# Kernel tuning notes

Measured on AMD Instinct MI355X. Metric: run time of the kernel, lower is better.

Reference implementation:

```python
import jax, jax.numpy as jnp
import numpy as np

D, H, BS, K_TOP = 2560, 32, 32, 16
HD = D // H  # 80
B, S = 2, 1024
SCALE = HD ** -0.5


def setup_inputs() -> dict:
    key = jax.random.key(0)
    ks = jax.random.split(key, 10)
    sc = 0.02

    def lin(k, i, o):
        return (jax.random.normal(k, (i, o), jnp.float32) * sc,
                jnp.zeros((o,), jnp.float32))

    Wq, bq = lin(ks[0], D, D)
    Wk, bk = lin(ks[1], D, D)
    Wv, bv = lin(ks[2], D, D)
    Wo, bo = lin(ks[3], D, D)
    comp_W1, comp_b1 = lin(ks[4], BS * HD, 4 * HD)
    comp_W2, comp_b2 = lin(ks[5], 4 * HD, HD)
    comp_pos = jax.random.normal(ks[6], (BS, HD), jnp.float32) * sc
    gate_W1, gate_b1 = lin(ks[7], D, D // 2)
    gate_W2, gate_b2 = lin(ks[8], D // 2, 3)
    hidden_states = jax.random.normal(ks[9], (B, S, D), jnp.float32)
    return dict(hidden_states=hidden_states, Wq=Wq, bq=bq, Wk=Wk, bk=bk,
                Wv=Wv, bv=bv, Wo=Wo, bo=bo, comp_pos=comp_pos,
                comp_W1=comp_W1, comp_b1=comp_b1, comp_W2=comp_W2,
                comp_b2=comp_b2, gate_W1=gate_W1, gate_b1=gate_b1,
                gate_W2=gate_W2, gate_b2=gate_b2)


def reference(hidden_states, Wq, bq, Wk, bk, Wv, bv, Wo, bo, comp_pos,
              comp_W1, comp_b1, comp_W2, comp_b2, gate_W1, gate_b1,
              gate_W2, gate_b2):
    b, s, dm = hidden_states.shape
    blocks = s // BS

    def heads(y):  # [b,s,D] -> [b,H,s,hd]
        return y.reshape(b, s, H, HD).transpose(0, 2, 1, 3)

    q = heads(hidden_states @ Wq + bq)
    k = heads(hidden_states @ Wk + bk)
    v = heads(hidden_states @ Wv + bv)

    # --- compression branch: per-head block compression MLP (shared K/V) ---
    def compress(t):  # [b,H,s,hd] -> [b,H,blocks,hd]
        tb = t.reshape(b, H, blocks, BS, HD) + comp_pos  # pos emb per block slot
        tb = tb.reshape(b, H, blocks, BS * HD)
        h1 = jax.nn.gelu(tb @ comp_W1 + comp_b1, approximate=False)
        return h1 @ comp_W2 + comp_b2

    kc = compress(k)
    vc = compress(v)
    attn_c = jax.nn.softmax(jnp.einsum('bhsd,bhnd->bhsn', q, kc) * SCALE, axis=-1)
    out_c = jnp.einsum('bhsn,bhnd->bhsd', attn_c, vc)

    # --- dense scores, shared by selection scoring and window branch ---
    scores = jnp.einsum('bhqd,bhkd->bhqk', q, k) * SCALE  # [b,H,s,s]

    # --- selection branch: per-query top-k blocks by block-mean score ---
    block_scores = scores.reshape(b, H, s, blocks, BS).mean(-1)  # [b,H,s,blocks]
    _, top_idx = jax.lax.top_k(block_scores, K_TOP)  # [b,H,s,K]
    sel = (jnp.arange(blocks)[None, None, None, None, :] == top_idx[..., None]).any(-2)
    key_mask = jnp.repeat(sel, BS, axis=-1)  # [b,H,s,s]
    sel_scores = jnp.where(key_mask, scores, -jnp.inf)
    out_s = jnp.einsum('bhqk,bhkd->bhqd', jax.nn.softmax(sel_scores, axis=-1), v)

    # --- window branch: source's window mask is all-ones -> full attention ---
    out_w = jnp.einsum('bhqk,bhkd->bhqd', jax.nn.softmax(scores, axis=-1), v)

    # --- learned gates ---
    gh = jax.nn.gelu(hidden_states @ gate_W1 + gate_b1, approximate=False)
    gates = jax.nn.sigmoid(gh @ gate_W2 + gate_b2)  # [b,s,3]
    g = gates.transpose(2, 0, 1)[:, :, None, :, None]  # [3,b,1,s,1]
    combined = g[0] * out_c + g[1] * out_s + g[2] * out_w  # [b,H,s,hd]
    combined = combined.transpose(0, 2, 1, 3).reshape(b, s, dm)
    return combined @ Wo + bo
```

## Files before the change

kernel.cpp:

```cpp
#include <hip/hip_runtime.h>
#include <hip/hip_bf16.h>
#include <math.h>

typedef unsigned short u16;
typedef short v8s __attribute__((ext_vector_type(8)));
typedef float v4f __attribute__((ext_vector_type(4)));

#define SCALE_F 0.11180339887498949f
#define SCALE_L2 0.16129821534f

__device__ __forceinline__ float bf2f(u16 x) {
    unsigned int u = ((unsigned int)x) << 16;
    return __builtin_bit_cast(float, u);
}
__device__ __forceinline__ u16 f2bf(float f) {
    unsigned int u = __builtin_bit_cast(unsigned int, f);
    unsigned int r = (u + 0x7FFFu + ((u >> 16) & 1u)) >> 16;
    return (u16)r;
}
__device__ __forceinline__ float scrub(float v) {
    return (fabsf(v) < 1e30f) ? v : 0.f;
}
__device__ __forceinline__ v8s zero8() {
    union { v8s v; short s[8]; } t;
#pragma unroll
    for (int i = 0; i < 8; i++) t.s[i] = 0;
    return t.v;
}
__device__ __forceinline__ void glds16(const void* g, void* s) {
    __builtin_amdgcn_global_load_lds(
        (const __attribute__((address_space(1))) unsigned int*)g,
        (__attribute__((address_space(3))) unsigned int*)s, 16, 0, 0);
}

__global__ void convX_kernel(const float* __restrict__ X, u16* __restrict__ Xb, int n)
{
    int i = (blockIdx.x * 256 + threadIdx.x) * 4;
    if (i >= n) return;
    float4 v = *(const float4*)(X + i);
    u16 o[4] = { f2bf(v.x), f2bf(v.y), f2bf(v.z), f2bf(v.w) };
    *(uint2*)(Xb + i) = *(uint2*)o;
}

__global__ __launch_bounds__(256) void convT_kernel(
    const float* __restrict__ W, u16* __restrict__ WT, int K, int N)
{
    __shared__ float t[32][33];
    int n0 = blockIdx.x * 32, k0 = blockIdx.y * 32;
    int tx = threadIdx.x & 31, ty = threadIdx.x >> 5;
    for (int i = ty; i < 32; i += 8) {
        int k = k0 + i, n = n0 + tx;
        t[i][tx] = (k < K && n < N) ? W[(size_t)k * N + n] : 0.f;
    }
    __syncthreads();
    for (int i = ty; i < 32; i += 8) {
        int n = n0 + i, k = k0 + tx;
        if (n < N && k < K) WT[(size_t)n * K + k] = f2bf(t[tx][i]);
    }
}

__global__ void xmean_kernel(const float* __restrict__ X, float* __restrict__ Xm)
{
    int c = blockIdx.x * 256 + threadIdx.x;
    if (c >= 2560) return;
    int g = blockIdx.y;
    const float* base = X + (size_t)g * 32 * 2560 + c;
    float s = 0.f;
#pragma unroll 4
    for (int j = 0; j < 32; j++) s += base[(size_t)j * 2560];
    Xm[(size_t)g * 2560 + c] = s * (1.f / 32.f);
}

__global__ __launch_bounds__(256) void gemmS_kernel(
    const float* __restrict__ A, const float* __restrict__ B,
    const float* __restrict__ bias, int M, int N, int K, float* __restrict__ outf)
{
    __shared__ __align__(16) u16 Ah[64][32], Al[64][32];
    __shared__ __align__(16) u16 Bh[64][32], Bl[64][32];
    const int tid = threadIdx.x;
    const int bm = blockIdx.x * 64, bn = blockIdx.y * 64;
    const int w = tid >> 6, lane = tid & 63;
    const int quad = lane >> 4, l = lane & 15;
    v4f acc[4];
#pragma unroll
    for (int nt = 0; nt < 4; nt++)
#pragma unroll
        for (int r = 0; r < 4; r++) acc[nt][r] = 0.f;
    const int ar = tid >> 2, ak = (tid & 3) * 8;
    const int kr = tid >> 3, nc = (tid & 7) * 8;
    for (int k0 = 0; k0 < K; k0 += 32) {
        float4 a0 = *(const float4*)(A + (size_t)(bm + ar) * K + (k0 + ak));
        float4 a1 = *(const float4*)(A + (size_t)(bm + ar) * K + (k0 + ak) + 4);
        float4 b0 = *(const float4*)(B + (size_t)(k0 + kr) * N + (bn + nc));
        float4 b1 = *(const float4*)(B + (size_t)(k0 + kr) * N + (bn + nc) + 4);
        float av[8] = {a0.x,a0.y,a0.z,a0.w,a1.x,a1.y,a1.z,a1.w};
        float bv[8] = {b0.x,b0.y,b0.z,b0.w,b1.x,b1.y,b1.z,b1.w};
        __syncthreads();
#pragma unroll
        for (int j = 0; j < 8; j++) {
            u16 h = f2bf(av[j]);
            Ah[ar][ak + j] = h; Al[ar][ak + j] = f2bf(av[j] - bf2f(h));
            u16 g = f2bf(bv[j]);
            Bh[nc + j][kr] = g; Bl[nc + j][kr] = f2bf(bv[j] - bf2f(g));
        }
        __syncthreads();
        v8s ah = *(const v8s*)(&Ah[w * 16 + l][quad * 8]);
        v8s al = *(const v8s*)(&Al[w * 16 + l][quad * 8]);
#pragma unroll
        for (int nt = 0; nt < 4; nt++) {
            v8s bh = *(const v8s*)(&Bh[nt * 16 + l][quad * 8]);
            v8s bl = *(const v8s*)(&Bl[nt * 16 + l][quad * 8]);
            acc[nt] = __builtin_amdgcn_mfma_f32_16x16x32_bf16(ah, bh, acc[nt], 0, 0, 0);
            acc[nt] = __builtin_amdgcn_mfma_f32_16x16x32_bf16(ah, bl, acc[nt], 0, 0, 0);
            acc[nt] = __builtin_amdgcn_mfma_f32_16x16x32_bf16(al, bh, acc[nt], 0, 0, 0);
        }
    }
#pragma unroll
    for (int nt = 0; nt < 4; nt++) {
        int col = bn + nt * 16 + l;
        float bvs = bias[col];
#pragma unroll
        for (int r = 0; r < 4; r++) {
            int row = bm + w * 16 + quad * 4 + r;
            outf[(size_t)row * N + col] = scrub(acc[nt][r] + bvs);
        }
    }
}

__global__ __launch_bounds__(256) void m1_kernel(
    const float* __restrict__ Wq, const float* __restrict__ km,
    u16* __restrict__ M1hT, u16* __restrict__ M1lT)
{
    __shared__ float Ws[64][81];
    __shared__ float Ks[32][80];
    int k0 = blockIdx.x * 64, h = blockIdx.y, b = blockIdx.z;
    int tid = threadIdx.x;
    for (int i = tid; i < 64 * 80; i += 256) {
        int kk = i / 80, dd = i - kk * 80;
        Ws[kk][dd] = Wq[(size_t)(k0 + kk) * 2560 + h * 80 + dd];
    }
    for (int i = tid; i < 32 * 80; i += 256) {
        int bl = i / 80, dd = i - bl * 80;
        Ks[bl][dd] = km[(size_t)((b << 5) + bl) * 2560 + h * 80 + dd];
    }
    __syncthreads();
    int kk = tid & 63, bq4 = tid >> 6;
    for (int bt = 0; bt < 8; bt++) {
        int blk = bt * 4 + bq4;
        float s = 0.f;
#pragma unroll 8
        for (int d = 0; d < 80; d++) s += Ws[kk][d] * Ks[blk][d];
        u16 hi = f2bf(s);
        size_t o = (size_t)(b * 1024 + h * 32 + blk) * 2560 + k0 + kk;
        M1hT[o] = hi;
        M1lT[o] = f2bf(s - bf2f(hi));
    }
}

__global__ void bias3_kernel(const float* __restrict__ bq, const float* __restrict__ km,
                             float* __restrict__ bias3)
{
    int i = blockIdx.x * 256 + threadIdx.x;
    if (i >= 2048) return;
    int b = i >> 10, hb = i & 1023, h = hb >> 5, blk = hb & 31;
    float s = 0.f;
    for (int d = 0; d < 80; d++) s += bq[h * 80 + d] * km[(size_t)((b << 5) + blk) * 2560 + h * 80 + d];
    bias3[i] = s;
}

__global__ __launch_bounds__(256) void gemmS2_kernel(
    const float* __restrict__ A, const u16* __restrict__ BhT, const u16* __restrict__ BlT,
    const float* __restrict__ bias, int M, int N, int K, float* __restrict__ outf)
{
    __shared__ __align__(16) u16 Ah[2][64][32], Al[2][64][32];
    __shared__ __align__(16) u16 Bh[2][64][32], Bl[2][64][32];
    const int tid = threadIdx.x;
    const int z = blockIdx.z;
    const float* Az = A + (size_t)z * 1024 * 2560;
    const u16* Bhz = BhT + (size_t)z * 1024 * 2560;
    const u16* Blz = BlT + (size_t)z * 1024 * 2560;
    const float* biasz = bias + (size_t)z * 1024;
    float* outz = outf + (size_t)z * 1024 * 1024;
    const int bm = blockIdx.x * 64, bn = blockIdx.y * 64;
    const int w = tid >> 6, lane = tid & 63;
    const int quad = lane >> 4, l = lane & 15;
    v4f acc[4];
#pragma unroll
    for (int nt = 0; nt < 4; nt++)
#pragma unroll
        for (int r = 0; r < 4; r++) acc[nt][r] = 0.f;
    const int ar = tid >> 2, ak = (tid & 3) * 8;
    const float* ApF = Az + (size_t)(bm + ar) * K + ak;
    const u16* BpH = Bhz + (size_t)(bn + ar) * K + ak;
    const u16* BpL = Blz + (size_t)(bn + ar) * K + ak;
    char* BhB = (char*)Bh;
    char* BlB = (char*)Bl;
    const int NT = K >> 5;
    glds16(BpH, BhB + w * 1024);
    glds16(BpL, BlB + w * 1024);
    float4 a0 = *(const float4*)(ApF);
    float4 a1 = *(const float4*)(ApF + 4);
    __syncthreads();
    for (int t = 0; t < NT; t++) {
        const int cur = t & 1;
        const int nxt = cur ^ 1;
        if (t + 1 < NT) {
            int k0n = (t + 1) << 5;
            glds16(BpH + k0n, BhB + nxt * 4096 + w * 1024);
            glds16(BpL + k0n, BlB + nxt * 4096 + w * 1024);
        }
        float av[8] = {a0.x, a0.y, a0.z, a0.w, a1.x, a1.y, a1.z, a1.w};
        if (t + 1 < NT) {
            int k0n = (t + 1) << 5;
            a0 = *(const float4*)(ApF + k0n);
            a1 = *(const float4*)(ApF + k0n + 4);
        }
#pragma unroll
        for (int j = 0; j < 8; j++) {
            u16 h = f2bf(av[j]);
            Ah[cur][ar][ak + j] = h;
            Al[cur][ar][ak + j] = f2bf(av[j] - bf2f(h));
        }
        v8s ah = *(const v8s*)(&Ah[cur][w * 16 + l][quad * 8]);
        v8s al2 = *(const v8s*)(&Al[cur][w * 16 + l][quad * 8]);
#pragma unroll
        for (int nt = 0; nt < 4; nt++) {
            v8s bh = *(const v8s*)(&Bh[cur][nt * 16 + l][quad * 8]);
            v8s bl = *(const v8s*)(&Bl[cur][nt * 16 + l][quad * 8]);
            acc[nt] = __builtin_amdgcn_mfma_f32_16x16x32_bf16(ah, bh, acc[nt], 0, 0, 0);
            acc[nt] = __builtin_amdgcn_mfma_f32_16x16x32_bf16(ah, bl, acc[nt], 0, 0, 0);
            acc[nt] = __builtin_amdgcn_mfma_f32_16x16x32_bf16(al2, bh, acc[nt], 0, 0, 0);
        }
        __syncthreads();
    }
#pragma unroll
    for (int nt = 0; nt < 4; nt++) {
        int col = bn + nt * 16 + l;
        float bvs = biasz[col];
#pragma unroll
        for (int r = 0; r < 4; r++) {
            int row = bm + w * 16 + quad * 4 + r;
            outz[(size_t)row * N + col] = scrub(acc[nt][r] + bvs);
        }
    }
}

__global__ __launch_bounds__(256) void gemmB_kernel(
    const u16* __restrict__ A, const u16* __restrict__ Al2, const u16* __restrict__ BT,
    const float* __restrict__ bias, int M, int N, int K, int act, int ldc,
    u16* __restrict__ outb, float* __restrict__ outf, u16* __restrict__ outT)
{
    __shared__ __align__(16) u16 As[2][64][32];
    __shared__ __align__(16) u16 As2[2][64][32];
    __shared__ __align__(16) u16 Bs[2][64][32];
    const int tid = threadIdx.x;
    const int bm = blockIdx.x * 64, bn = blockIdx.y * 64;
    const int w = tid >> 6, lane = tid & 63;
    const int quad = lane >> 4, l = lane & 15;
    v4f acc[4];
#pragma unroll
    for (int nt = 0; nt < 4; nt++)
#pragma unroll
        for (int r = 0; r < 4; r++) acc[nt][r] = 0.f;
    const int srow = w * 16 + (lane >> 2);
    const int kcol = (lane & 3) * 8;
    const int brow = (bn + srow < N) ? (bn + srow) : (N - 1);
    const u16* Ap = A + (size_t)(bm + srow) * K + kcol;
    const u16* Bp = BT + (size_t)brow * K + kcol;
    const u16* A2p = Al2 ? (Al2 + (size_t)(bm + srow) * K + kcol) : nullptr;
    char* AsB = (char*)As;
    char* As2B = (char*)As2;
    char* BsB = (char*)Bs;
    const int NT = K >> 5;
    glds16(Ap, AsB + w * 1024);
    glds16(Bp, BsB + w * 1024);
    if (Al2) glds16(A2p, As2B + w * 1024);
    __syncthreads();
    for (int t = 0; t < NT; t++) {
        const int cur = t & 1;
        const int nxt = cur ^ 1;
        if (t + 1 < NT) {
            int k0n = (t + 1) << 5;
            glds16(Ap + k0n, AsB + nxt * 4096 + w * 1024);
            glds16(Bp + k0n, BsB + nxt * 4096 + w * 1024);
            if (Al2) glds16(A2p + k0n, As2B + nxt * 4096 + w * 1024);
        }
        v8s af = *(const v8s*)(&As[cur][w * 16 + l][quad * 8]);
#pragma unroll
        for (int nt = 0; nt < 4; nt++) {
            v8s bf = *(const v8s*)(&Bs[cur][nt * 16 + l][quad * 8]);
            acc[nt] = __builtin_amdgcn_mfma_f32_16x16x32_bf16(af, bf, acc[nt], 0, 0, 0);
        }
        if (Al2) {
            v8s af2 = *(const v8s*)(&As2[cur][w * 16 + l][quad * 8]);
#pragma unroll
            for (int nt = 0; nt < 4; nt++) {
                v8s bf = *(const v8s*)(&Bs[cur][nt * 16 + l][quad * 8]);
                acc[nt] = __builtin_amdgcn_mfma_f32_16x16x32_bf16(af2, bf, acc[nt], 0, 0, 0);
            }
        }
        __syncthreads();
    }
#pragma unroll
    for (int nt = 0; nt < 4; nt++) {
        int col = bn + nt * 16 + l;
        if (col < N) {
            float bvs = bias[col];
#pragma unroll
            for (int r = 0; r < 4; r++) {
                int row = bm + w * 16 + quad * 4 + r;
                float c = acc[nt][r] + bvs;
                if (act == 1) c = 0.5f * c * (1.0f + erff(c * 0.70710678118654752f));
                c = scrub(c);
                if (outf) outf[(size_t)row * ldc + col] = c;
                if (outb) outb[(size_t)row * ldc + col] = f2bf(c);
                if (outT) {
                    int bb = row >> 10, s = row & 1023;
                    int hh = col / 80, dd = col - hh * 80;
                    outT[((size_t)((bb << 5) + hh) * 96 + dd) * 1024 + s] = f2bf(c);
                }
            }
        }
    }
}

__global__ void gatherF_kernel(const u16* __restrict__ src, const float* __restrict__ pos,
                               u16* __restrict__ F)
{
    int row = blockIdx.y;
    int col = blockIdx.x * 256 + threadIdx.x;
    if (col >= 2560) return;
    int b = row >> 10, h = (row >> 5) & 31, blk = row & 31;
    int j = col / 80, d = col - j * 80;
    float v = bf2f(src[(size_t)(b * 1024 + blk * 32 + j) * 2560 + h * 80 + d]) + pos[col];
    F[(size_t)row * 2560 + col] = f2bf(v);
}
__global__ void gatherFT_kernel(const u16* __restrict__ vt, const float* __restrict__ pos,
                                u16* __restrict__ F)
{
    int row = blockIdx.y;
    int col = blockIdx.x * 256 + threadIdx.x;
    if (col >= 2560) return;
    int b = row >> 10, h = (row >> 5) & 31, blk = row & 31;
    int j = col / 80, d = col - j * 80;
    float v = bf2f(vt[((size_t)((b << 5) + h) * 96 + d) * 1024 + blk * 32 + j]) + pos[col];
    F[(size_t)row * 2560 + col] = f2bf(v);
}

__global__ __launch_bounds__(256) void gates_kernel(
    const u16* __restrict__ gh, const float* __restrict__ W2,
    const float* __restrict__ b2, float* __restrict__ gates)
{
    int w = threadIdx.x >> 6, lane = threadIdx.x & 63;
    int token = blockIdx.x * 4 + w;
    float s0 = 0.f, s1 = 0.f, s2 = 0.f;
    for (int i = lane; i < 1280; i += 64) {
        float g = bf2f(gh[(size_t)token * 1280 + i]);
        s0 += g * W2[i * 3 + 0];
        s1 += g * W2[i * 3 + 1];
        s2 += g * W2[i * 3 + 2];
    }
#pragma unroll
    for (int m = 1; m < 64; m <<= 1) {
        s0 += __shfl_xor(s0, m);
        s1 += __shfl_xor(s1, m);
        s2 += __shfl_xor(s2, m);
    }
    if (lane == 0) {
        gates[token * 3 + 0] = scrub(1.f / (1.f + expf(-(s0 + b2[0]))));
        gates[token * 3 + 1] = scrub(1.f / (1.f + expf(-(s1 + b2[1]))));
        gates[token * 3 + 2] = scrub(1.f / (1.f + expf(-(s2 + b2[2]))));
    }
}

__global__ __launch_bounds__(64) void attn_kernel(
    const u16* __restrict__ qb, const u16* __restrict__ kbf,
    const u16* __restrict__ vt, const u16* __restrict__ kc,
    const u16* __restrict__ vc, const float* __restrict__ BSf,
    const float* __restrict__ gates, u16* __restrict__ comb, u16* __restrict__ combl)
{
    const int lane = threadIdx.x, quad = lane >> 4, l = lane & 15;
    const int qt = blockIdx.x, bh = blockIdx.y, b = bh >> 5, h = bh & 31;
    const float NEG = -1e30f;

    __shared__ float bs[16][33];
    __shared__ unsigned int selmask[16];
    __shared__ __align__(16) u16 Pw[16][40];
    __shared__ float ocn[16][80];

    {
        const float* bsrow = BSf + ((size_t)b * 1024 + qt * 16 + l) * 1024 + h * 32 + quad * 8;
#pragma unroll
        for (int i = 0; i < 8; i++) bs[l][quad * 8 + i] = bsrow[i] * SCALE_F;
    }
    __syncthreads();
    if (lane < 16) {
        unsigned int mask = 0u;
        for (int it = 0; it < 16; it++) {
            float best = NEG; int bi = -1;
            for (int n = 0; n < 32; n++) {
                if (((mask >> n) & 1u) == 0u && bs[lane][n] > best) { best = bs[lane][n]; bi = n; }
            }
            if (bi < 0) { for (int n = 0; n < 32; n++) if (((mask >> n) & 1u) == 0u) { bi = n; break; } }
            mask |= (1u << bi);
        }
        selmask[lane] = mask;
    }
    __syncthreads();
    const unsigned int selm_l = selmask[l];
    unsigned int selm[4];
#pragma unroll
    for (int r = 0; r < 4; r++) selm[r] = selmask[quad * 4 + r];

    v8s qfrag[3];
    {
        const u16* qrow = qb + (size_t)(b * 1024 + qt * 16 + l) * 2560 + h * 80;
#pragma unroll
        for (int c = 0; c < 3; c++) {
            if (c == 2 && quad >= 2) { qfrag[c] = zero8(); }
            else qfrag[c] = *(const v8s*)(qrow + c * 32 + quad * 8);
        }
    }

    {
        v4f oc[5];
#pragma unroll
        for (int t = 0; t < 5; t++)
#pragma unroll
            for (int r = 0; r < 4; r++) oc[t][r] = 0.f;
        float l_c[4];
        v4f s0, s1;
#pragma unroll
        for (int r = 0; r < 4; r++) { s0[r] = 0.f; s1[r] = 0.f; }
#pragma unroll
        for (int c = 0; c < 3; c++) {
            v8s b0, b1;
            if (c == 2 && quad >= 2) { b0 = zero8(); b1 = zero8(); }
            else {
                b0 = *(const v8s*)(kc + (size_t)(bh * 32 + l) * 80 + c * 32 + quad * 8);
                b1 = *(const v8s*)(kc + (size_t)(bh * 32 + 16 + l) * 80 + c * 32 + quad * 8);
            }
            s0 = __builtin_amdgcn_mfma_f32_16x16x32_bf16(qfrag[c], b0, s0, 0, 0, 0);
            s1 = __builtin_amdgcn_mfma_f32_16x16x32_bf16(qfrag[c], b1, s1, 0, 0, 0);
        }
#pragma unroll
        for (int r = 0; r < 4; r++) {
            float x0 = s0[r] * SCALE_L2, x1 = s1[r] * SCALE_L2;
            float mx = fmaxf(x0, x1);
#pragma unroll
            for (int m = 1; m < 16; m <<= 1) mx = fmaxf(mx, __shfl_xor(mx, m));
            float p0 = exp2f(x0 - mx), p1 = exp2f(x1 - mx);
            float sm = p0 + p1;
#pragma unroll
            for (int m = 1; m < 16; m <<= 1) sm += __shfl_xor(sm, m);
            l_c[r] = sm;
            Pw[quad * 4 + r][l]      = f2bf(p0);
            Pw[quad * 4 + r][l + 16] = f2bf(p1);
        }
        __syncthreads();
        v8s pa = *(const v8s*)(&Pw[l][quad * 8]);
#pragma unroll
        for (int t = 0; t < 5; t++) {
            union { v8s v; short s[8]; } vf;
#pragma unroll
            for (int j = 0; j < 8; j++)
                vf.s[j] = (short)vc[(size_t)(bh * 32 + quad * 8 + j) * 80 + t * 16 + l];
            oc[t] = __builtin_amdgcn_mfma_f32_16x16x32_bf16(pa, vf.v, oc[t], 0, 0, 0);
        }
#pragma unroll
        for (int r = 0; r < 4; r++) {
            int token = b * 1024 + qt * 16 + quad * 4 + r;
            float g0 = gates[token * 3 + 0];
            float fc = g0 / fmaxf(l_c[r], 1e-30f);
#pragma unroll
            for (int t = 0; t < 5; t++) ocn[quad * 4 + r][t * 16 + l] = oc[t][r] * fc;
        }
        __syncthreads();
    }

    v4f aw[5], as_[5];
    float m_w[4], l_w[4], l_s[4];
#pragma unroll
    for (int r = 0; r < 4; r++) { m_w[r] = NEG; l_w[r] = 0.f; l_s[r] = 0.f; }
#pragma unroll
    for (int t = 0; t < 5; t++)
#pragma unroll
        for (int r = 0; r < 4; r++) { aw[t][r] = 0.f; as_[t][r] = 0.f; }

    const u16* vtp = vt + (size_t)bh * 96 * 1024;

    for (int kb = 0; kb < 32; kb++) {
        v4f s0, s1;
#pragma unroll
        for (int r = 0; r < 4; r++) { s0[r] = 0.f; s1[r] = 0.f; }
#pragma unroll
        for (int c = 0; c < 3; c++) {
            v8s k0f, k1f;
            if (c == 2 && quad >= 2) { k0f = zero8(); k1f = zero8(); }
            else {
                size_t base = (size_t)(b * 1024 + kb * 32) * 2560 + h * 80 + c * 32 + quad * 8;
                k0f = *(const v8s*)(kbf + base + (size_t)l * 2560);
                k1f = *(const v8s*)(kbf + base + (size_t)(16 + l) * 2560);
            }
            s0 = __builtin_amdgcn_mfma_f32_16x16x32_bf16(qfrag[c], k0f, s0, 0, 0, 0);
            s1 = __builtin_amdgcn_mfma_f32_16x16x32_bf16(qfrag[c], k1f, s1, 0, 0, 0);
        }
        float x0a[4], x1a[4], pmax[4];
        float needmax = NEG;
#pragma unroll
        for (int r = 0; r < 4; r++) {
            x0a[r] = s0[r] * SCALE_L2; x1a[r] = s1[r] * SCALE_L2;
            float mb = fmaxf(x0a[r], x1a[r]);
#pragma unroll
            for (int m = 1; m < 16; m <<= 1) mb = fmaxf(mb, __shfl_xor(mb, m));
            pmax[r] = mb;
            needmax = fmaxf(needmax, mb - m_w[r]);
        }
        if (__all(needmax <= 8.0f)) {
#pragma unroll
            for (int r = 0; r < 4; r++) {
                float p0 = exp2f(x0a[r] - m_w[r]), p1 = exp2f(x1a[r] - m_w[r]);
                Pw[quad * 4 + r][l]      = f2bf(p0);
                Pw[quad * 4 + r][l + 16] = f2bf(p1);
                float st = p0 + p1;
#pragma unroll
                for (int m = 1; m < 16; m <<= 1) st += __shfl_xor(st, m);
                l_w[r] += st;
                if ((selm[r] >> kb) & 1u) l_s[r] += st;
            }
        } else {
            float alw[4];
#pragma unroll
            for (int r = 0; r < 4; r++) {
                float mn = fmaxf(m_w[r], pmax[r]);
                alw[r] = exp2f(m_w[r] - mn);
                m_w[r] = mn;
                float p0 = exp2f(x0a[r] - mn), p1 = exp2f(x1a[r] - mn);
                Pw[quad * 4 + r][l]      = f2bf(p0);
                Pw[quad * 4 + r][l + 16] = f2bf(p1);
                float st = p0 + p1;
#pragma unroll
                for (int m = 1; m < 16; m <<= 1) st += __shfl_xor(st, m);
                l_w[r] = l_w[r] * alw[r] + st;
                l_s[r] = l_s[r] * alw[r] + (((selm[r] >> kb) & 1u) ? st : 0.f);
            }
#pragma unroll
            for (int t = 0; t < 5; t++)
#pragma unroll
                for (int r = 0; r < 4; r++) { aw[t][r] *= alw[r]; as_[t][r] *= alw[r]; }
        }
        __syncthreads();
        v8s pwa = *(const v8s*)(&Pw[l][quad * 8]);
        v8s psa = ((selm_l >> kb) & 1u) ? pwa : zero8();
#pragma unroll
        for (int t = 0; t < 5; t++) {
            v8s vfr = *(const v8s*)(vtp + ((size_t)(t * 16 + l)) * 1024 + kb * 32 + quad * 8);
            aw[t]  = __builtin_amdgcn_mfma_f32_16x16x32_bf16(pwa, vfr, aw[t], 0, 0, 0);
            as_[t] = __builtin_amdgcn_mfma_f32_16x16x32_bf16(psa, vfr, as_[t], 0, 0, 0);
        }
        __syncthreads();
    }

#pragma unroll
    for (int r = 0; r < 4; r++) {
        int token = b * 1024 + qt * 16 + quad * 4 + r;
        float g1 = gates[token * 3 + 1], g2 = gates[token * 3 + 2];
        float fw = g2 / fmaxf(l_w[r], 1e-30f);
        float fs = g1 / fmaxf(l_s[r], 1e-30f);
#pragma unroll
        for (int t = 0; t < 5; t++) {
            float val = ocn[quad * 4 + r][t * 16 + l] + fs * as_[t][r] + fw * aw[t][r];
            val = scrub(val);
            u16 hi = f2bf(val);
            size_t o = (size_t)token * 2560 + h * 80 + t * 16 + l;
            comb[o] = hi;
            combl[o] = f2bf(val - bf2f(hi));
        }
    }
}

extern "C" void kernel_launch(void* const* d_in, const int* in_sizes, int n_in,
                              void* d_out, int out_size, void* d_ws, size_t ws_size,
                              hipStream_t stream)
{
    (void)in_sizes; (void)n_in; (void)out_size; (void)ws_size;

    const float* X   = (const float*)d_in[0];
    const float* Wq  = (const float*)d_in[1];
    const float* bq  = (const float*)d_in[2];
    const float* Wk  = (const float*)d_in[3];
    const float* bk  = (const float*)d_in[4];
    const float* Wv  = (const float*)d_in[5];
    const float* bv  = (const float*)d_in[6];
    const float* Wo  = (const float*)d_in[7];
    const float* bo  = (const float*)d_in[8];
    const float* pos = (const float*)d_in[9];
    const float* cW1 = (const float*)d_in[10];
    const float* cb1 = (const float*)d_in[11];
    const float* cW2 = (const float*)d_in[12];
    const float* cb2 = (const float*)d_in[13];
    const float* gW1 = (const float*)d_in[14];
    const float* gb1 = (const float*)d_in[15];
    const float* gW2 = (const float*)d_in[16];
    const float* gb2 = (const float*)d_in[17];

    char* ws = (char*)d_ws;
    size_t off = 0;
    auto alloc = [&](size_t bytes) -> void* {
        void* p = ws + off;
        off += (bytes + 255) & ~(size_t)255;
        return p;
    };
    u16*   Xb     = (u16*)  alloc(2048ull * 2560 * 2);
    u16*   WqT    = (u16*)  alloc(2560ull * 2560 * 2);
    u16*   WkT    = (u16*)  alloc(2560ull * 2560 * 2);
    u16*   WvT    = (u16*)  alloc(2560ull * 2560 * 2);
    u16*   WoT    = (u16*)  alloc(2560ull * 2560 * 2);
    u16*   gW1T   = (u16*)  alloc(1280ull * 2560 * 2);
    u16*   cW1T   = (u16*)  alloc(320ull * 2560 * 2);
    u16*   cW2T   = (u16*)  alloc(96ull * 320 * 2);
    float* Xm     = (float*)alloc(64ull * 2560 * 4);
    float* kmeanS = (float*)alloc(64ull * 2560 * 4);
    u16*   M1hT   = (u16*)  alloc(2048ull * 2560 * 2);
    u16*   M1lT   = (u16*)  alloc(2048ull * 2560 * 2);
    float* bias3  = (float*)alloc(2048ull * 4);
    u16*   qbuf   = (u16*)  alloc(2048ull * 2560 * 2);
    u16*   kbf    = (u16*)  alloc(2048ull * 2560 * 2);
    u16*   vtb    = (u16*)  alloc(64ull * 96 * 1024 * 2);
    u16*   combl  = (u16*)  alloc(2048ull * 2560 * 2);
    char*  R1     = (char*) alloc(12ull * 1024 * 1024);
    u16*   gh     = (u16*)R1;
    u16*   Fb     = (u16*)R1;
    u16*   H1     = (u16*)(R1 + 10ull * 1024 * 1024);
    u16*   combb  = (u16*)R1;
    u16*   KC     = (u16*)  alloc(2048ull * 80 * 2);
    u16*   VC     = (u16*)  alloc(2048ull * 80 * 2);
    float* gatesf = (float*)alloc(2048ull * 3 * 4);
    float* BSf    = (float*)d_out;

    dim3 blk(256);
    convX_kernel<<<2048 * 2560 / 4 / 256, blk, 0, stream>>>(X, Xb, 2048 * 2560);
    convT_kernel<<<dim3(80, 80), blk, 0, stream>>>(Wq, WqT, 2560, 2560);
    convT_kernel<<<dim3(80, 80), blk, 0, stream>>>(Wk, WkT, 2560, 2560);
    convT_kernel<<<dim3(80, 80), blk, 0, stream>>>(Wv, WvT, 2560, 2560);
    convT_kernel<<<dim3(80, 80), blk, 0, stream>>>(Wo, WoT, 2560, 2560);
    convT_kernel<<<dim3(40, 80), blk, 0, stream>>>(gW1, gW1T, 2560, 1280);
    convT_kernel<<<dim3(10, 80), blk, 0, stream>>>(cW1, cW1T, 2560, 320);
    convT_kernel<<<dim3(3, 10), blk, 0, stream>>>(cW2, cW2T, 320, 80);
    xmean_kernel<<<dim3(10, 64), blk, 0, stream>>>(X, Xm);
    gemmS_kernel<<<dim3(1, 40), blk, 0, stream>>>(Xm, Wk, bk, 64, 2560, 2560, kmeanS);
    m1_kernel<<<dim3(40, 32, 2), blk, 0, stream>>>(Wq, kmeanS, M1hT, M1lT);
    bias3_kernel<<<8, blk, 0, stream>>>(bq, kmeanS, bias3);
    gemmS2_kernel<<<dim3(16, 16, 2), blk, 0, stream>>>(X, M1hT, M1lT, bias3, 1024, 1024, 2560, BSf);
    gemmB_kernel<<<dim3(32, 40), blk, 0, stream>>>(Xb, nullptr, WqT, bq, 2048, 2560, 2560, 0, 2560, qbuf, nullptr, nullptr);
    gemmB_kernel<<<dim3(32, 40), blk, 0, stream>>>(Xb, nullptr, WkT, bk, 2048, 2560, 2560, 0, 2560, kbf, nullptr, nullptr);
    gemmB_kernel<<<dim3(32, 40), blk, 0, stream>>>(Xb, nullptr, WvT, bv, 2048, 2560, 2560, 0, 2560, nullptr, nullptr, vtb);
    gemmB_kernel<<<dim3(32, 20), blk, 0, stream>>>(Xb, nullptr, gW1T, gb1, 2048, 1280, 2560, 1, 1280, gh, nullptr, nullptr);
    gates_kernel<<<512, blk, 0, stream>>>(gh, gW2, gb2, gatesf);
    gatherF_kernel<<<dim3(10, 2048), blk, 0, stream>>>(kbf, pos, Fb);
    gemmB_kernel<<<dim3(32, 5), blk, 0, stream>>>(Fb, nullptr, cW1T, cb1, 2048, 320, 2560, 1, 320, H1, nullptr, nullptr);
    gemmB_kernel<<<dim3(32, 2), blk, 0, stream>>>(H1, nullptr, cW2T, cb2, 2048, 80, 320, 0, 80, KC, nullptr, nullptr);
    gatherFT_kernel<<<dim3(10, 2048), blk, 0, stream>>>(vtb, pos, Fb);
    gemmB_kernel<<<dim3(32, 5), blk, 0, stream>>>(Fb, nullptr, cW1T, cb1, 2048, 320, 2560, 1, 320, H1, nullptr, nullptr);
    gemmB_kernel<<<dim3(32, 2), blk, 0, stream>>>(H1, nullptr, cW2T, cb2, 2048, 80, 320, 0, 80, VC, nullptr, nullptr);
    attn_kernel<<<dim3(64, 64), 64, 0, stream>>>(qbuf, kbf, vtb, KC, VC, BSf, gatesf, combb, combl);
    gemmB_kernel<<<dim3(32, 40), blk, 0, stream>>>(combb, combl, WoT, bo, 2048, 2560, 2560, 0, 2560, nullptr, (float*)d_out, nullptr);
}
```

Baseline: 1.137 ms.

## Software-pipeline K loads, hoist V loads, and drop single-wavefront barriers in attention

The attention key loop is unrolled by two with ping-pong register buffers, so the K fragments for the next block are loaded while the current block's softmax runs. The five V fragments are issued at the start of each iteration, ahead of the QK MFMAs. Every __syncthreads is removed on the basis that the block is a single 64-lane wavefront. This is meant to hide global-memory latency and cut barrier overhead, at the cost of more live registers and a reliance on implicit wavefront-level ordering of LDS accesses.

```diff
diff --git a/kernel.cpp b/kernel.cpp
--- a/kernel.cpp
+++ b/kernel.cpp
@@ -373,6 +373,94 @@
     }
 }
 
+#define KLOAD(K0,K1,K2,K3,K4,K5, kbv) do {                                    \
+    size_t base_ = (size_t)(b * 1024 + (kbv) * 32) * 2560 + h * 80 + quad * 8;\
+    const u16* p0_ = kbf + base_ + (size_t)l * 2560;                          \
+    const u16* p1_ = kbf + base_ + (size_t)(16 + l) * 2560;                   \
+    K0 = *(const v8s*)(p0_);                                                  \
+    K1 = *(const v8s*)(p0_ + 32);                                             \
+    K3 = *(const v8s*)(p1_);                                                  \
+    K4 = *(const v8s*)(p1_ + 32);                                             \
+    if (quad < 2) { K2 = *(const v8s*)(p0_ + 64); K5 = *(const v8s*)(p1_ + 64); } \
+    else { K2 = zero8(); K5 = zero8(); }                                      \
+} while (0)
+
+#define ATTN_ITER(kbv, K0,K1,K2,K3,K4,K5, DOPRE, N0,N1,N2,N3,N4,N5) do {      \
+    const int kb_ = (kbv);                                                    \
+    const u16* vp_ = vtp + kb_ * 32 + quad * 8;                               \
+    v8s va0_ = *(const v8s*)(vp_ + (size_t)(l) * 1024);                       \
+    v8s va1_ = *(const v8s*)(vp_ + (size_t)(16 + l) * 1024);                  \
+    v8s va2_ = *(const v8s*)(vp_ + (size_t)(32 + l) * 1024);                  \
+    v8s va3_ = *(const v8s*)(vp_ + (size_t)(48 + l) * 1024);                  \
+    v8s va4_ = *(const v8s*)(vp_ + (size_t)(64 + l) * 1024);                  \
+    v4f s0_, s1_;                                                             \
+    _Pragma("unroll")                                                         \
+    for (int r = 0; r < 4; r++) { s0_[r] = 0.f; s1_[r] = 0.f; }               \
+    s0_ = __builtin_amdgcn_mfma_f32_16x16x32_bf16(qfrag[0], K0, s0_, 0, 0, 0);\
+    s0_ = __builtin_amdgcn_mfma_f32_16x16x32_bf16(qfrag[1], K1, s0_, 0, 0, 0);\
+    s0_ = __builtin_amdgcn_mfma_f32_16x16x32_bf16(qfrag[2], K2, s0_, 0, 0, 0);\
+    s1_ = __builtin_amdgcn_mfma_f32_16x16x32_bf16(qfrag[0], K3, s1_, 0, 0, 0);\
+    s1_ = __builtin_amdgcn_mfma_f32_16x16x32_bf16(qfrag[1], K4, s1_, 0, 0, 0);\
+    s1_ = __builtin_amdgcn_mfma_f32_16x16x32_bf16(qfrag[2], K5, s1_, 0, 0, 0);\
+    if (DOPRE) { KLOAD(N0, N1, N2, N3, N4, N5, kb_ + 1); }                    \
+    float x0a_[4], x1a_[4], pmax_[4];                                         \
+    float needmax_ = NEG;                                                     \
+    _Pragma("unroll")                                                         \
+    for (int r = 0; r < 4; r++) {                                             \
+        x0a_[r] = s0_[r] * SCALE_L2; x1a_[r] = s1_[r] * SCALE_L2;             \
+        float mb_ = fmaxf(x0a_[r], x1a_[r]);                                  \
+        _Pragma("unroll")                                                     \
+        for (int m = 1; m < 16; m <<= 1) mb_ = fmaxf(mb_, __shfl_xor(mb_, m));\
+        pmax_[r] = mb_;                                                       \
+        needmax_ = fmaxf(needmax_, mb_ - m_w[r]);                             \
+    }                                                                         \
+    if (__all(needmax_ <= 8.0f)) {                                            \
+        _Pragma("unroll")                                                     \
+        for (int r = 0; r < 4; r++) {                                         \
+            float p0_ = exp2f(x0a_[r] - m_w[r]), p1_ = exp2f(x1a_[r] - m_w[r]); \
+            Pw[quad * 4 + r][l]      = f2bf(p0_);                             \
+            Pw[quad * 4 + r][l + 16] = f2bf(p1_);                             \
+            float st_ = p0_ + p1_;                                            \
+            _Pragma("unroll")                                                 \
+            for (int m = 1; m < 16; m <<= 1) st_ += __shfl_xor(st_, m);       \
+            l_w[r] += st_;                                                    \
+            if ((selm[r] >> kb_) & 1u) l_s[r] += st_;                         \
+        }                                                                     \
+    } else {                                                                  \
+        float alw_[4];                                                        \
+        _Pragma("unroll")                                                     \
+        for (int r = 0; r < 4; r++) {                                         \
+            float mn_ = fmaxf(m_w[r], pmax_[r]);                              \
+            alw_[r] = exp2f(m_w[r] - mn_);                                    \
+            m_w[r] = mn_;                                                     \
+            float p0_ = exp2f(x0a_[r] - mn_), p1_ = exp2f(x1a_[r] - mn_);     \
+            Pw[quad * 4 + r][l]      = f2bf(p0_);                             \
+            Pw[quad * 4 + r][l + 16] = f2bf(p1_);                             \
+            float st_ = p0_ + p1_;                                            \
+            _Pragma("unroll")                                                 \
+            for (int m = 1; m < 16; m <<= 1) st_ += __shfl_xor(st_, m);       \
+            l_w[r] = l_w[r] * alw_[r] + st_;                                  \
+            l_s[r] = l_s[r] * alw_[r] + (((selm[r] >> kb_) & 1u) ? st_ : 0.f);\
+        }                                                                     \
+        _Pragma("unroll")                                                     \
+        for (int t = 0; t < 5; t++)                                           \
+            _Pragma("unroll")                                                 \
+            for (int r = 0; r < 4; r++) { aw[t][r] *= alw_[r]; as_[t][r] *= alw_[r]; } \
+    }                                                                         \
+    v8s pwa_ = *(const v8s*)(&Pw[l][quad * 8]);                               \
+    v8s psa_ = ((selm_l >> kb_) & 1u) ? pwa_ : zero8();                       \
+    aw[0]  = __builtin_amdgcn_mfma_f32_16x16x32_bf16(pwa_, va0_, aw[0], 0, 0, 0); \
+    as_[0] = __builtin_amdgcn_mfma_f32_16x16x32_bf16(psa_, va0_, as_[0], 0, 0, 0); \
+    aw[1]  = __builtin_amdgcn_mfma_f32_16x16x32_bf16(pwa_, va1_, aw[1], 0, 0, 0); \
+    as_[1] = __builtin_amdgcn_mfma_f32_16x16x32_bf16(psa_, va1_, as_[1], 0, 0, 0); \
+    aw[2]  = __builtin_amdgcn_mfma_f32_16x16x32_bf16(pwa_, va2_, aw[2], 0, 0, 0); \
+    as_[2] = __builtin_amdgcn_mfma_f32_16x16x32_bf16(psa_, va2_, as_[2], 0, 0, 0); \
+    aw[3]  = __builtin_amdgcn_mfma_f32_16x16x32_bf16(pwa_, va3_, aw[3], 0, 0, 0); \
+    as_[3] = __builtin_amdgcn_mfma_f32_16x16x32_bf16(psa_, va3_, as_[3], 0, 0, 0); \
+    aw[4]  = __builtin_amdgcn_mfma_f32_16x16x32_bf16(pwa_, va4_, aw[4], 0, 0, 0); \
+    as_[4] = __builtin_amdgcn_mfma_f32_16x16x32_bf16(psa_, va4_, as_[4], 0, 0, 0); \
+} while (0)
+
 __global__ __launch_bounds__(64) void attn_kernel(
     const u16* __restrict__ qb, const u16* __restrict__ kbf,
     const u16* __restrict__ vt, const u16* __restrict__ kc,
@@ -393,7 +481,6 @@
 #pragma unroll
         for (int i = 0; i < 8; i++) bs[l][quad * 8 + i] = bsrow[i] * SCALE_F;
     }
-    __syncthreads();
     if (lane < 16) {
         unsigned int mask = 0u;
         for (int it = 0; it < 16; it++) {
@@ -406,7 +493,6 @@
         }
         selmask[lane] = mask;
     }
-    __syncthreads();
     const unsigned int selm_l = selmask[l];
     unsigned int selm[4];
 #pragma unroll
@@ -457,7 +543,6 @@
             Pw[quad * 4 + r][l]      = f2bf(p0);
             Pw[quad * 4 + r][l + 16] = f2bf(p1);
         }
-        __syncthreads();
         v8s pa = *(const v8s*)(&Pw[l][quad * 8]);
 #pragma unroll
         for (int t = 0; t < 5; t++) {
@@ -475,7 +560,6 @@
 #pragma unroll
             for (int t = 0; t < 5; t++) ocn[quad * 4 + r][t * 16 + l] = oc[t][r] * fc;
         }
-        __syncthreads();
     }
 
     v4f aw[5], as_[5];
@@ -489,76 +573,16 @@
 
     const u16* vtp = vt + (size_t)bh * 96 * 1024;
 
-    for (int kb = 0; kb < 32; kb++) {
-        v4f s0, s1;
-#pragma unroll
-        for (int r = 0; r < 4; r++) { s0[r] = 0.f; s1[r] = 0.f; }
-#pragma unroll
-        for (int c = 0; c < 3; c++) {
-            v8s k0f, k1f;
-            if (c == 2 && quad >= 2) { k0f = zero8(); k1f = zero8(); }
-            else {
-                size_t base = (size_t)(b * 1024 + kb * 32) * 2560 + h * 80 + c * 32 + quad * 8;
-                k0f = *(const v8s*)(kbf + base + (size_t)l * 2560);
-                k1f = *(const v8s*)(kbf + base + (size_t)(16 + l) * 2560);
-            }
-            s0 = __builtin_amdgcn_mfma_f32_16x16x32_bf16(qfrag[c], k0f, s0, 0, 0, 0);
-            s1 = __builtin_amdgcn_mfma_f32_16x16x32_bf16(qfrag[c], k1f, s1, 0, 0, 0);
-        }
-        float x0a[4], x1a[4], pmax[4];
-        float needmax = NEG;
-#pragma unroll
-        for (int r = 0; r < 4; r++) {
-            x0a[r] = s0[r] * SCALE_L2; x1a[r] = s1[r] * SCALE_L2;
-            float mb = fmaxf(x0a[r], x1a[r]);
-#pragma unroll
-            for (int m = 1; m < 16; m <<= 1) mb = fmaxf(mb, __shfl_xor(mb, m));
-            pmax[r] = mb;
-            needmax = fmaxf(needmax, mb - m_w[r]);
-        }
-        if (__all(needmax <= 8.0f)) {
-#pragma unroll
-            for (int r = 0; r < 4; r++) {
-                float p0 = exp2f(x0a[r] - m_w[r]), p1 = exp2f(x1a[r] - m_w[r]);
-                Pw[quad * 4 + r][l]      = f2bf(p0);
-                Pw[quad * 4 + r][l + 16] = f2bf(p1);
-                float st = p0 + p1;
-#pragma unroll
-                for (int m = 1; m < 16; m <<= 1) st += __shfl_xor(st, m);
-                l_w[r] += st;
-                if ((selm[r] >> kb) & 1u) l_s[r] += st;
-            }
-        } else {
-            float alw[4];
-#pragma unroll
-            for (int r = 0; r < 4; r++) {
-                float mn = fmaxf(m_w[r], pmax[r]);
-                alw[r] = exp2f(m_w[r] - mn);
-                m_w[r] = mn;
-                float p0 = exp2f(x0a[r] - mn), p1 = exp2f(x1a[r] - mn);
-                Pw[quad * 4 + r][l]      = f2bf(p0);
-                Pw[quad * 4 + r][l + 16] = f2bf(p1);
-                float st = p0 + p1;
-#pragma unroll
-                for (int m = 1; m < 16; m <<= 1) st += __shfl_xor(st, m);
-                l_w[r] = l_w[r] * alw[r] + st;
-                l_s[r] = l_s[r] * alw[r] + (((selm[r] >> kb) & 1u) ? st : 0.f);
-            }
-#pragma unroll
-            for (int t = 0; t < 5; t++)
-#pragma unroll
-                for (int r = 0; r < 4; r++) { aw[t][r] *= alw[r]; as_[t][r] *= alw[r]; }
-        }
-        __syncthreads();
-        v8s pwa = *(const v8s*)(&Pw[l][quad * 8]);
-        v8s psa = ((selm_l >> kb) & 1u) ? pwa : zero8();
-#pragma unroll
-        for (int t = 0; t < 5; t++) {
-            v8s vfr = *(const v8s*)(vtp + ((size_t)(t * 16 + l)) * 1024 + kb * 32 + quad * 8);
-            aw[t]  = __builtin_amdgcn_mfma_f32_16x16x32_bf16(pwa, vfr, aw[t], 0, 0, 0);
-            as_[t] = __builtin_amdgcn_mfma_f32_16x16x32_bf16(psa, vfr, as_[t], 0, 0, 0);
-        }
-        __syncthreads();
+    v8s ka0, ka1, ka2, ka3, ka4, ka5;
+    v8s kn0 = zero8(), kn1 = zero8(), kn2 = zero8(),
+        kn3 = zero8(), kn4 = zero8(), kn5 = zero8();
+    KLOAD(ka0, ka1, ka2, ka3, ka4, ka5, 0);
+
+    for (int kb2 = 0; kb2 < 32; kb2 += 2) {
+        ATTN_ITER(kb2,     ka0, ka1, ka2, ka3, ka4, ka5, true,
+                           kn0, kn1, kn2, kn3, kn4, kn5);
+        ATTN_ITER(kb2 + 1, kn0, kn1, kn2, kn3, kn4, kn5, (kb2 + 2 < 32),
+                           ka0, ka1, ka2, ka3, ka4, ka5);
     }
 
 #pragma unroll
```

After: 1.203 ms. +5.8%, slower.
